# Optimization experiments

Measured on AMD Instinct MI355X. Metric: run time of the kernel, lower is better.

The kernel has to match this reference:

```python
import jax, jax.numpy as jnp
import numpy as np

# Llama-3-8B-ish config + NSA defaults from the adapter
H, KVH, DH = 32, 8, 128
D = H * DH            # 4096 hidden
CB = 16               # compress block size (stride == block -> non-overlapping)
SB = 16               # selection block size
NSEL = 4              # num selected blocks
WIN = 64              # sliding window size
B, S = 1, 1024
NEG = -jnp.finfo(jnp.float32).max


def rope(x):
    # interleaved rotary (rotary_embedding_torch default, theta=10000); x: [b,h,n,d]
    b, h, n, d = x.shape
    inv = 1.0 / (10000.0 ** (jnp.arange(0, d, 2, dtype=jnp.float32) / d))
    ang = jnp.arange(n, dtype=jnp.float32)[:, None] * inv[None, :]      # [n, d/2]
    cos, sin = jnp.cos(ang), jnp.sin(ang)
    xr = x.reshape(b, h, n, d // 2, 2)
    x0, x1 = xr[..., 0], xr[..., 1]
    o0 = x0 * cos - x1 * sin
    o1 = x1 * cos + x0 * sin
    return jnp.stack([o0, o1], axis=-1).reshape(b, h, n, d)


def nsa_forward(hidden_states, w_qkv, w_o, k_pos, v_pos,
                k_w1, k_b1, k_w2, k_b2, v_w1, v_b1, v_w2, v_b2,
                mem_kv, w_gate, b_gate):
    Bq, Sq = hidden_states.shape[:2]
    G = H // KVH
    scale = DH ** -0.5

    qkv = hidden_states @ w_qkv.T
    q, k, v = jnp.split(qkv, [H * DH, H * DH + KVH * DH], axis=-1)
    q = q.reshape(Bq, Sq, H, DH).transpose(0, 2, 1, 3)     # b h s d
    k = k.reshape(Bq, Sq, KVH, DH).transpose(0, 2, 1, 3)   # b kvh s d
    v = v.reshape(Bq, Sq, KVH, DH).transpose(0, 2, 1, 3)

    # ---- branch 1: compressed (coarse) attention ------------------------
    nC = Sq // CB
    kp = jnp.tile(k_pos, (1, nC, 1))[None]                 # intra-block learned positions
    vp = jnp.tile(v_pos, (1, nC, 1))[None]
    ck_in = (k + kp).reshape(Bq, KVH, nC, CB * DH)
    cv_in = (v + vp).reshape(Bq, KVH, nC, CB * DH)
    ck = jax.nn.relu(ck_in @ k_w1.T + k_b1) @ k_w2.T + k_b2   # b kvh nC d
    cv = jax.nn.relu(cv_in @ v_w1.T + v_b1) @ v_w2.T + v_b2
    mem_k = jnp.broadcast_to(mem_kv[0], (Bq, KVH, 1, DH))
    mem_v = jnp.broadcast_to(mem_kv[1], (Bq, KVH, 1, DH))
    ck = jnp.concatenate([mem_k, ck], axis=2)              # b kvh (1+nC) d
    cv = jnp.concatenate([mem_v, cv], axis=2)

    qg = q.reshape(Bq, KVH, G, Sq, DH)
    csim = jnp.einsum('bhgid,bhjd->bhgij', qg, ck) * scale
    ck_seq = jnp.concatenate([jnp.array([-1]), (jnp.arange(nC) + 1) * CB - 1])
    cmask = ck_seq[None, :] < jnp.arange(Sq)[:, None]      # [S, 1+nC], mem always visible
    csim = jnp.where(cmask, csim, NEG)
    c_out = jnp.einsum('bhgij,bhjd->bhgid', jax.nn.softmax(csim, -1), cv)
    c_out = c_out.reshape(Bq, H, Sq, DH)

    # ---- importance scores -> top-k selected blocks ---------------------
    imp = csim[..., 1:].mean(axis=2)                       # mean over grouped q heads: b kvh s nC
    sent = jnp.full(imp.shape[:-1] + (1,), -1e3, imp.dtype)
    imp = jax.nn.softmax(jnp.concatenate([sent, imp], -1), -1)[..., 1:]
    sel_val, sel_idx = jax.lax.top_k(imp, NSEL)            # b kvh s NSEL
    fmask_sel = sel_val > 1e-10

    rq, rk = rope(q), rope(k)

    # ---- branch 2: fine attention over selected + own (block-causal) block
    own = jnp.arange(Sq) // SB
    sel_idx = jnp.concatenate(
        [sel_idx, jnp.broadcast_to(own, (Bq, KVH, Sq))[..., None]], axis=-1)  # b kvh s (NSEL+1)
    nF = Sq // SB
    fk_b = rk.reshape(Bq, KVH, nF, SB, DH)
    fv_b = v.reshape(Bq, KVH, nF, SB, DH)
    bi = jnp.arange(Bq)[:, None, None, None]
    hi = jnp.arange(KVH)[None, :, None, None]
    fk = fk_b[bi, hi, sel_idx].reshape(Bq, KVH, Sq, (NSEL + 1) * SB, DH)
    fv = fv_b[bi, hi, sel_idx].reshape(Bq, KVH, Sq, (NSEL + 1) * SB, DH)

    diag = jnp.arange(SB)[None, :] <= (jnp.arange(Sq) % SB)[:, None]   # [S, SB]
    fmask = jnp.concatenate(
        [jnp.broadcast_to(fmask_sel[..., None], (Bq, KVH, Sq, NSEL, SB)),
         jnp.broadcast_to(diag, (Bq, KVH, Sq, SB))[..., None, :]], axis=3)
    fmask = fmask.reshape(Bq, KVH, 1, Sq, (NSEL + 1) * SB)

    fq = rq.reshape(Bq, KVH, G, Sq, DH)
    fsim = jnp.einsum('bhgid,bhijd->bhgij', fq, fk) * scale
    fsim = jnp.where(fmask, fsim, NEG)
    f_out = jnp.einsum('bhgij,bhijd->bhgid', jax.nn.softmax(fsim, -1), fv)
    f_out = f_out.reshape(Bq, H, Sq, DH)

    # ---- branch 3: sliding window (exact window, look_backward=1) -------
    sk = jnp.repeat(rk, G, axis=1)                          # b H s d
    sv = jnp.repeat(v, G, axis=1)
    nW = Sq // WIN
    sqw = rq.reshape(Bq, H, nW, WIN, DH)
    skw = sk.reshape(Bq, H, nW, WIN, DH)
    svw = sv.reshape(Bq, H, nW, WIN, DH)
    pad5 = ((0, 0), (0, 0), (1, 0), (0, 0), (0, 0))
    skc = jnp.concatenate([jnp.pad(skw, pad5)[:, :, :nW], skw], axis=3)  # prev + own window
    svc = jnp.concatenate([jnp.pad(svw, pad5)[:, :, :nW], svw], axis=3)
    rel = (WIN + jnp.arange(WIN))[:, None] - jnp.arange(2 * WIN)[None, :]  # i_abs - j_abs
    band = (rel >= 0) & (rel <= WIN)
    key_abs = jnp.arange(nW)[:, None] * WIN + jnp.arange(2 * WIN)[None, :] - WIN
    smask = band[None] & (key_abs >= 0)[:, None, :]
    ssim = jnp.einsum('bhwid,bhwjd->bhwij', sqw, skc) * scale
    ssim = jnp.where(smask, ssim, NEG)
    s_out = jnp.einsum('bhwij,bhwjd->bhwid', jax.nn.softmax(ssim, -1), svc)
    s_out = s_out.reshape(Bq, H, Sq, DH)

    # ---- learned 3-way gate + output projection --------------------------
    gates = jax.nn.sigmoid(hidden_states @ w_gate.T + b_gate)
    gates = gates.reshape(Bq, Sq, H, 3).transpose(0, 2, 1, 3)  # b h s 3
    out = gates[..., 0:1] * c_out + gates[..., 1:2] * f_out + gates[..., 2:3] * s_out
    out = out.transpose(0, 2, 1, 3).reshape(Bq, Sq, H * DH)
    return out @ w_o.T


def setup_inputs():
    key = jax.random.key(0)
    ks = jax.random.split(key, 12)
    cdim = CB * DH
    rn = lambda k, shape, s: jax.random.normal(k, shape, dtype=jnp.float32) * s
    return {
        'hidden_states': rn(ks[0], (B, S, D), 1.0),
        'w_qkv': rn(ks[1], (H * DH + 2 * KVH * DH, D), D ** -0.5),
        'w_o': rn(ks[2], (D, H * DH), D ** -0.5),
        'k_pos': rn(ks[3], (KVH, CB, DH), 0.02),
        'v_pos': rn(ks[4], (KVH, CB, DH), 0.02),
        'k_w1': rn(ks[5], (cdim, cdim), cdim ** -0.5),
        'k_b1': jnp.zeros((cdim,), jnp.float32),
        'k_w2': rn(ks[6], (DH, cdim), cdim ** -0.5),
        'k_b2': jnp.zeros((DH,), jnp.float32),
        'v_w1': rn(ks[7], (cdim, cdim), cdim ** -0.5),
        'v_b1': jnp.zeros((cdim,), jnp.float32),
        'v_w2': rn(ks[8], (DH, cdim), cdim ** -0.5),
        'v_b2': jnp.zeros((DH,), jnp.float32),
        'mem_kv': rn(ks[9], (2, KVH, 1, DH), 0.02),
        'w_gate': rn(ks[10], (3 * H, D), 0.02),
        'b_gate': jnp.tile(jnp.array([-2.0, -2.0, 2.0], jnp.float32), H),
    }


def reference(hidden_states, w_qkv, w_o, k_pos, v_pos,
              k_w1, k_b1, k_w2, k_b2, v_w1, v_b1, v_w2, v_b2,
              mem_kv, w_gate, b_gate):
    return nsa_forward(hidden_states, w_qkv, w_o, k_pos, v_pos,
                       k_w1, k_b1, k_w2, k_b2, v_w1, v_b1, v_w2, v_b2,
                       mem_kv, w_gate, b_gate)
```

## Files before the change

kernel.cpp:

```cpp
#include <hip/hip_runtime.h>
#include <hip/hip_bf16.h>

typedef __hip_bfloat16 bf16;
typedef __attribute__((ext_vector_type(8))) short short8;
typedef __attribute__((ext_vector_type(4))) float f32x4;

#define NEGF (-3.402823466e38f)
#define SCALE 0.08838834764831845f

constexpr int S_    = 1024;
constexpr int H_    = 32;
constexpr int KVH_  = 8;
constexpr int DH_   = 128;
constexpr int QKVN  = 6144;
constexpr int NC_   = 64;
constexpr int CD_   = 2048;

__device__ __forceinline__ short f2bf(float x) {
    union { float f; unsigned u; } v; v.f = x;
    unsigned r = v.u + 0x7fffu + ((v.u >> 16) & 1u);
    return (short)(r >> 16);
}
__device__ __forceinline__ float bf2f(short h) {
    union { float f; unsigned u; } v; v.u = ((unsigned)(unsigned short)h) << 16;
    return v.f;
}

#define GLOAD16(gp, lp) __builtin_amdgcn_global_load_lds( \
    (const __attribute__((address_space(1))) unsigned int*)(gp), \
    (__attribute__((address_space(3))) unsigned int*)(lp), 16, 0, 0)

__global__ void split_pair(const float* __restrict__ src, short* __restrict__ h,
                           short* __restrict__ l, long n)
{
    long i = ((long)blockIdx.x * blockDim.x + threadIdx.x) * 8;
    if (i >= n) return;
    float4 a0 = *(const float4*)&src[i];
    float4 a1 = *(const float4*)&src[i + 4];
    float e[8] = {a0.x, a0.y, a0.z, a0.w, a1.x, a1.y, a1.z, a1.w};
    short8 hh, ll;
    #pragma unroll
    for (int j = 0; j < 8; ++j) {
        short hv = f2bf(e[j]); hh[j] = hv; ll[j] = f2bf(e[j] - bf2f(hv));
    }
    *(short8*)&h[i] = hh;
    *(short8*)&l[i] = ll;
}

__global__ __launch_bounds__(64)
void gemm_w64(const short* __restrict__ Ah, const short* __restrict__ Al,
              const short* __restrict__ Bh, const short* __restrict__ Bl,
              float* __restrict__ C, float* __restrict__ Cpart,
              const float* __restrict__ bias,
              int M, int N, int K, int ldc, int k_len, int act)
{
    __shared__ short LA[2][2][2048];
    __shared__ short LB[2][2][2048];
    const int lane = threadIdx.x;
    const int qd = lane >> 4, l16 = lane & 15;
    const int bm = blockIdx.y * 64, bn = blockIdx.x * 64;
    const int kbeg = blockIdx.z * k_len;
    const int kend = (kbeg + k_len < K) ? (kbeg + k_len) : K;

    const int srow = lane >> 2, skq = lane & 3;
    const short* gAh = Ah + (size_t)(bm + srow) * K + skq * 8;
    const short* gAl = Al + (size_t)(bm + srow) * K + skq * 8;
    const short* gBh = Bh + (size_t)(bn + srow) * K + skq * 8;
    const short* gBl = Bl + (size_t)(bn + srow) * K + skq * 8;

    #define STAGE(buf, kk) do {                                         \
        _Pragma("unroll")                                               \
        for (int c = 0; c < 4; ++c) {                                   \
            size_t go = (size_t)c * 16 * K + (kk);                      \
            GLOAD16(gAh + go, &LA[buf][0][c * 512]);                    \
            GLOAD16(gAl + go, &LA[buf][1][c * 512]);                    \
            GLOAD16(gBh + go, &LB[buf][0][c * 512]);                    \
            GLOAD16(gBl + go, &LB[buf][1][c * 512]);                    \
        } } while (0)

    f32x4 zero = {0.f, 0.f, 0.f, 0.f};
    f32x4 acc[4][4];
    #pragma unroll
    for (int i = 0; i < 4; ++i)
        #pragma unroll
        for (int j = 0; j < 4; ++j) acc[i][j] = zero;

    STAGE(0, kbeg);
    int cur = 0;
    for (int k0 = kbeg; k0 < kend; k0 += 32) {
        if (k0 + 32 < kend) {
            STAGE(cur ^ 1, k0 + 32);
            asm volatile("s_waitcnt vmcnt(16)" ::: "memory");
        } else {
            asm volatile("s_waitcnt vmcnt(0)" ::: "memory");
        }
        short8 fah[4], fal[4], fbh[4], fbl[4];
        #pragma unroll
        for (int t = 0; t < 4; ++t) {
            int off = t * 512 + l16 * 32 + qd * 8;
            fah[t] = *(const short8*)&LA[cur][0][off];
            fal[t] = *(const short8*)&LA[cur][1][off];
            fbh[t] = *(const short8*)&LB[cur][0][off];
            fbl[t] = *(const short8*)&LB[cur][1][off];
        }
        __builtin_amdgcn_s_setprio(1);
        #pragma unroll
        for (int t = 0; t < 4; ++t)
            #pragma unroll
            for (int u = 0; u < 4; ++u) {
                acc[t][u] = __builtin_amdgcn_mfma_f32_16x16x32_bf16(fah[t], fbh[u], acc[t][u], 0, 0, 0);
                acc[t][u] = __builtin_amdgcn_mfma_f32_16x16x32_bf16(fah[t], fbl[u], acc[t][u], 0, 0, 0);
                acc[t][u] = __builtin_amdgcn_mfma_f32_16x16x32_bf16(fal[t], fbh[u], acc[t][u], 0, 0, 0);
            }
        __builtin_amdgcn_s_setprio(0);
        cur ^= 1;
    }
    #undef STAGE

    float* dst = Cpart ? (Cpart + (size_t)blockIdx.z * M * ldc) : C;
    #pragma unroll
    for (int t = 0; t < 4; ++t) {
        #pragma unroll
        for (int u = 0; u < 4; ++u) {
            int row0 = bm + t * 16 + qd * 4;
            int col  = bn + u * 16 + l16;
            #pragma unroll
            for (int r = 0; r < 4; ++r) {
                float v = acc[t][u][r];
                if (!Cpart) {
                    if (bias) v += bias[col];
                    if (act == 1) v = fmaxf(v, 0.f);
                    else if (act == 2) v = 1.f / (1.f + expf(-v));
                }
                dst[(size_t)(row0 + r) * ldc + col] = v;
            }
        }
    }
}

__global__ __launch_bounds__(256)
void gemm128(const float* __restrict__ A, const float* __restrict__ B,
             float* __restrict__ C, float* __restrict__ Cpart,
             const float* __restrict__ bias,
             int M, int N, int K, int k_len, int act)
{
    __shared__ float As[16][132];
    __shared__ float Bs[16][132];
    const int tid  = threadIdx.x;
    const int wave = tid >> 6, lane = tid & 63;
    const int wr = wave >> 1, wc = wave & 1;
    const int ro = wr * 64 + (lane >> 3) * 8;
    const int co = wc * 64 + (lane & 7) * 8;
    const int bm = blockIdx.y * 128, bn = blockIdx.x * 128;
    const int z  = blockIdx.z;
    const int kbeg = z * k_len;
    const int lr = tid >> 2;
    const int kq = (tid & 3) * 4;

    float acc[8][8];
    #pragma unroll
    for (int i = 0; i < 8; ++i)
        #pragma unroll
        for (int j = 0; j < 8; ++j) acc[i][j] = 0.f;

    for (int k0 = kbeg; k0 < kbeg + k_len; k0 += 16) {
        #pragma unroll
        for (int h = 0; h < 2; ++h) {
            int r = lr + h * 64;
            float4 av = make_float4(0.f, 0.f, 0.f, 0.f);
            float4 bv = make_float4(0.f, 0.f, 0.f, 0.f);
            if (bm + r < M) av = *(const float4*)&A[(size_t)(bm + r) * K + k0 + kq];
            if (bn + r < N) bv = *(const float4*)&B[(size_t)(bn + r) * K + k0 + kq];
            As[kq + 0][r] = av.x; As[kq + 1][r] = av.y;
            As[kq + 2][r] = av.z; As[kq + 3][r] = av.w;
            Bs[kq + 0][r] = bv.x; Bs[kq + 1][r] = bv.y;
            Bs[kq + 2][r] = bv.z; Bs[kq + 3][r] = bv.w;
        }
        __syncthreads();
        #pragma unroll
        for (int kk = 0; kk < 16; ++kk) {
            float4 a0 = *(const float4*)&As[kk][ro];
            float4 a1 = *(const float4*)&As[kk][ro + 4];
            float4 b0 = *(const float4*)&Bs[kk][co];
            float4 b1 = *(const float4*)&Bs[kk][co + 4];
            float a[8] = {a0.x, a0.y, a0.z, a0.w, a1.x, a1.y, a1.z, a1.w};
            float b[8] = {b0.x, b0.y, b0.z, b0.w, b1.x, b1.y, b1.z, b1.w};
            #pragma unroll
            for (int i = 0; i < 8; ++i)
                #pragma unroll
                for (int j = 0; j < 8; ++j)
                    acc[i][j] += a[i] * b[j];
        }
        __syncthreads();
    }

    if (Cpart) {
        float* P = Cpart + (size_t)z * M * N;
        #pragma unroll
        for (int i = 0; i < 8; ++i) {
            int row = bm + ro + i;
            #pragma unroll
            for (int jq = 0; jq < 2; ++jq) {
                int col = bn + co + jq * 4;
                if (col < N) {
                    float4 v = make_float4(acc[i][jq * 4 + 0], acc[i][jq * 4 + 1],
                                           acc[i][jq * 4 + 2], acc[i][jq * 4 + 3]);
                    *(float4*)&P[(size_t)row * N + col] = v;
                }
            }
        }
    } else {
        #pragma unroll
        for (int i = 0; i < 8; ++i) {
            int row = bm + ro + i;
            #pragma unroll
            for (int jq = 0; jq < 2; ++jq) {
                int col = bn + co + jq * 4;
                if (col < N) {
                    float4 v = make_float4(acc[i][jq * 4 + 0], acc[i][jq * 4 + 1],
                                           acc[i][jq * 4 + 2], acc[i][jq * 4 + 3]);
                    if (bias) {
                        float4 bv = *(const float4*)&bias[col];
                        v.x += bv.x; v.y += bv.y; v.z += bv.z; v.w += bv.w;
                    }
                    if (act == 1) {
                        v.x = fmaxf(v.x, 0.f); v.y = fmaxf(v.y, 0.f);
                        v.z = fmaxf(v.z, 0.f); v.w = fmaxf(v.w, 0.f);
                    } else if (act == 2) {
                        v.x = 1.f / (1.f + expf(-v.x)); v.y = 1.f / (1.f + expf(-v.y));
                        v.z = 1.f / (1.f + expf(-v.z)); v.w = 1.f / (1.f + expf(-v.w));
                    }
                    *(float4*)&C[(size_t)row * N + col] = v;
                }
            }
        }
    }
}

__global__ void reduce_slices(const float* __restrict__ P, float* __restrict__ C,
                              short* __restrict__ Chi, short* __restrict__ Clo,
                              const float* __restrict__ bias,
                              int MN, int N, int KS, int act)
{
    int i4 = blockIdx.x * blockDim.x + threadIdx.x;
    size_t base = (size_t)i4 * 4;
    if (base >= (size_t)MN) return;
    float4 s = *(const float4*)&P[base];
    for (int z = 1; z < KS; ++z) {
        float4 v = *(const float4*)&P[(size_t)z * MN + base];
        s.x += v.x; s.y += v.y; s.z += v.z; s.w += v.w;
    }
    if (bias) {
        int col = (int)(base % N);
        float4 bv = *(const float4*)&bias[col];
        s.x += bv.x; s.y += bv.y; s.z += bv.z; s.w += bv.w;
    }
    if (act == 1) {
        s.x = fmaxf(s.x, 0.f); s.y = fmaxf(s.y, 0.f);
        s.z = fmaxf(s.z, 0.f); s.w = fmaxf(s.w, 0.f);
    } else if (act == 2) {
        s.x = 1.f / (1.f + expf(-s.x)); s.y = 1.f / (1.f + expf(-s.y));
        s.z = 1.f / (1.f + expf(-s.z)); s.w = 1.f / (1.f + expf(-s.w));
    }
    if (Chi) {
        float e[4] = {s.x, s.y, s.z, s.w};
        short4 hh, ll;
        hh.x = f2bf(e[0]); ll.x = f2bf(e[0] - bf2f(hh.x));
        hh.y = f2bf(e[1]); ll.y = f2bf(e[1] - bf2f(hh.y));
        hh.z = f2bf(e[2]); ll.z = f2bf(e[2] - bf2f(hh.z));
        hh.w = f2bf(e[3]); ll.w = f2bf(e[3] - bf2f(hh.w));
        *(short4*)&Chi[base] = hh;
        *(short4*)&Clo[base] = ll;
    } else {
        *(float4*)&C[base] = s;
    }
}

__global__ void build_cin(const float* __restrict__ qkv,
                          const float* __restrict__ k_pos,
                          const float* __restrict__ v_pos,
                          short* __restrict__ ckh, short* __restrict__ ckl,
                          short* __restrict__ cvh, short* __restrict__ cvl)
{
    int idx = blockIdx.x * blockDim.x + threadIdx.x;
    if (idx >= KVH_ * S_ * DH_) return;
    int d = idx & 127;
    int s = (idx >> 7) & 1023;
    int h = idx >> 17;
    int c = s >> 4, t = s & 15;
    float kv = qkv[(size_t)s * QKVN + 4096 + h * DH_ + d];
    float vv = qkv[(size_t)s * QKVN + 5120 + h * DH_ + d];
    size_t row = (size_t)h * NC_ + c;
    size_t col = (size_t)t * DH_ + d;
    float kx = kv + k_pos[(h * 16 + t) * DH_ + d];
    float vx = vv + v_pos[(h * 16 + t) * DH_ + d];
    short kh = f2bf(kx), vh = f2bf(vx);
    ckh[row * CD_ + col] = kh; ckl[row * CD_ + col] = f2bf(kx - bf2f(kh));
    cvh[row * CD_ + col] = vh; cvl[row * CD_ + col] = f2bf(vx - bf2f(vh));
}

__global__ void assemble_c(const float* __restrict__ ckb, const float* __restrict__ cvb,
                           const float* __restrict__ mem_kv,
                           float* __restrict__ ckf, float* __restrict__ cvf)
{
    int idx = blockIdx.x * blockDim.x + threadIdx.x;
    if (idx >= KVH_ * 65 * DH_) return;
    int d = idx & 127;
    int j = (idx >> 7) % 65;
    int h = idx / (65 * DH_);
    if (j == 0) {
        ckf[idx] = mem_kv[(0 * KVH_ + h) * DH_ + d];
        cvf[idx] = mem_kv[(1 * KVH_ + h) * DH_ + d];
    } else {
        ckf[idx] = ckb[((size_t)h * NC_ + (j - 1)) * DH_ + d];
        cvf[idx] = cvb[((size_t)h * NC_ + (j - 1)) * DH_ + d];
    }
}

__global__ void compress_attn(const float* __restrict__ qkv,
                              const float* __restrict__ ckf,
                              const float* __restrict__ cvf,
                              float* __restrict__ cout,
                              int* __restrict__ selidx, int* __restrict__ fsel)
{
    int b = blockIdx.x;
    int s = b & 1023;
    int h = b >> 10;
    int tid = threadIdx.x;
    int wv = tid >> 6;
    __shared__ __align__(16) float qrow[4][128];
    __shared__ float simS[4][65];
    __shared__ float p[4][128];
    __shared__ float redm[2][4], redd[2][4];
    #pragma unroll
    for (int g = 0; g < 4; ++g)
        qrow[g][tid] = qkv[(size_t)s * QKVN + (h * 4 + g) * DH_ + tid];
    __syncthreads();

    float sv[4] = {NEGF, NEGF, NEGF, NEGF};
    if (tid < 65) {
        bool vis = (tid == 0) || (16 * tid - 1 < s);
        if (vis) {
            const float4* kr = (const float4*)(ckf + ((size_t)h * 65 + tid) * DH_);
            float a[4] = {0.f, 0.f, 0.f, 0.f};
            #pragma unroll 4
            for (int d = 0; d < 32; ++d) {
                float4 kq = kr[d];
                #pragma unroll
                for (int g = 0; g < 4; ++g) {
                    float4 qq = *(const float4*)&qrow[g][d * 4];
                    a[g] += kq.x * qq.x + kq.y * qq.y + kq.z * qq.z + kq.w * qq.w;
                }
            }
            #pragma unroll
            for (int g = 0; g < 4; ++g) sv[g] = a[g] * SCALE;
        }
        #pragma unroll
        for (int g = 0; g < 4; ++g) simS[g][tid] = sv[g];
    }

    float mg[4];
    #pragma unroll
    for (int g = 0; g < 4; ++g) mg[g] = sv[g];
    #pragma unroll
    for (int off = 32; off; off >>= 1)
        #pragma unroll
        for (int g = 0; g < 4; ++g) mg[g] = fmaxf(mg[g], __shfl_xor(mg[g], off));
    if ((tid & 63) == 0)
        #pragma unroll
        for (int g = 0; g < 4; ++g) redm[wv][g] = mg[g];
    __syncthreads();
    float e[4];
    #pragma unroll
    for (int g = 0; g < 4; ++g) {
        float m = fmaxf(redm[0][g], redm[1][g]);
        e[g] = (tid < 65) ? expf(sv[g] - m) : 0.f;
        p[g][tid] = e[g];
    }
    __syncthreads();
    #pragma unroll
    for (int off = 32; off; off >>= 1)
        #pragma unroll
        for (int g = 0; g < 4; ++g) e[g] += __shfl_xor(e[g], off);
    if ((tid & 63) == 0)
        #pragma unroll
        for (int g = 0; g < 4; ++g) redd[wv][g] = e[g];
    __syncthreads();
    float inv[4];
    #pragma unroll
    for (int g = 0; g < 4; ++g) inv[g] = 1.f / (redd[0][g] + redd[1][g]);

    if (wv == 1) {
        int j = tid - 64;
        float v = 0.25f * (simS[0][j + 1] + simS[1][j + 1] +
                           simS[2][j + 1] + simS[3][j + 1]);
        float m2 = v;
        #pragma unroll
        for (int off = 32; off; off >>= 1) m2 = fmaxf(m2, __shfl_xor(m2, off));
        m2 = fmaxf(m2, -1e3f);
        float e2 = expf(v - m2);
        float den2 = e2;
        #pragma unroll
        for (int off = 32; off; off >>= 1) den2 += __shfl_xor(den2, off);
        den2 += expf(-1e3f - m2);
        float pv = e2 / den2;
        size_t base5 = ((size_t)h * S_ + s) * 5;
        size_t base4 = ((size_t)h * S_ + s) * 4;
        float cv = pv; int ci = j;
        for (int t = 0; t < 4; ++t) {
            float bv = cv; int bi = ci;
            #pragma unroll
            for (int off = 32; off; off >>= 1) {
                float ov = __shfl_xor(bv, off);
                int   oi = __shfl_xor(bi, off);
                if (ov > bv || (ov == bv && oi < bi)) { bv = ov; bi = oi; }
            }
            if (j == 0) {
                selidx[base5 + t] = bi;
                fsel[base4 + t]   = (bv > 1e-10f) ? 1 : 0;
            }
            if (ci == bi) cv = -1.f;
        }
        if (j == 0) selidx[base5 + 4] = s >> 4;
    }

    float acc[4] = {0.f, 0.f, 0.f, 0.f};
    const float* vbase = cvf + (size_t)h * 65 * DH_ + tid;
    #pragma unroll 4
    for (int j = 0; j < 65; ++j) {
        float v = vbase[(size_t)j * DH_];
        #pragma unroll
        for (int g = 0; g < 4; ++g) acc[g] += p[g][j] * v;
    }
    #pragma unroll
    for (int g = 0; g < 4; ++g)
        cout[(size_t)s * 4096 + (h * 4 + g) * DH_ + tid] = acc[g] * inv[g];
}

__global__ void rope_inplace(float* __restrict__ qkv)
{
    int idx = blockIdx.x * blockDim.x + threadIdx.x;
    const int totq = S_ * H_ * 64;
    const int totk = S_ * KVH_ * 64;
    float* base;
    int p, s;
    if (idx < totq) {
        p = idx & 63; int head = (idx >> 6) & 31; s = idx >> 11;
        base = qkv + (size_t)s * QKVN + head * DH_;
    } else {
        int i2 = idx - totq;
        if (i2 >= totk) return;
        p = i2 & 63; int head = (i2 >> 6) & 7; s = i2 >> 9;
        base = qkv + (size_t)s * QKVN + 4096 + head * DH_;
    }
    float inv = exp2f(-0.2076205060833595f * (float)p);
    float ang = (float)s * inv;
    float c = cosf(ang), sn = sinf(ang);
    float x0 = base[2 * p], x1 = base[2 * p + 1];
    base[2 * p]     = x0 * c - x1 * sn;
    base[2 * p + 1] = x1 * c + x0 * sn;
}

__global__ void fine_attn(const float* __restrict__ qkv,
                          const int* __restrict__ selidx, const int* __restrict__ fsel,
                          float* __restrict__ fout)
{
    int b = blockIdx.x;
    int s = b & 1023;
    int h = b >> 10;
    int tid = threadIdx.x;
    int wv = tid >> 6;
    __shared__ __align__(16) float qrow[4][128];
    __shared__ float p[4][128];
    __shared__ int   blk[5];
    __shared__ int   bvis[5];
    __shared__ float redm[2][4], redd[2][4];
    if (tid < 5) {
        blk[tid]  = selidx[((size_t)h * S_ + s) * 5 + tid];
        bvis[tid] = (tid < 4) ? fsel[((size_t)h * S_ + s) * 4 + tid] : 1;
    }
    #pragma unroll
    for (int g = 0; g < 4; ++g)
        qrow[g][tid] = qkv[(size_t)s * QKVN + (h * 4 + g) * DH_ + tid];
    __syncthreads();

    float sv[4] = {NEGF, NEGF, NEGF, NEGF};
    if (tid < 80) {
        int bi = tid >> 4, t = tid & 15;
        int pos = blk[bi] * 16 + t;
        bool vis = (bi < 4) ? (bvis[bi] != 0) : (t <= (s & 15));
        if (vis) {
            const float4* kr = (const float4*)(qkv + (size_t)pos * QKVN + 4096 + h * DH_);
            float a[4] = {0.f, 0.f, 0.f, 0.f};
            #pragma unroll 4
            for (int d = 0; d < 32; ++d) {
                float4 kq = kr[d];
                #pragma unroll
                for (int g = 0; g < 4; ++g) {
                    float4 qq = *(const float4*)&qrow[g][d * 4];
                    a[g] += kq.x * qq.x + kq.y * qq.y + kq.z * qq.z + kq.w * qq.w;
                }
            }
            #pragma unroll
            for (int g = 0; g < 4; ++g) sv[g] = a[g] * SCALE;
        }
    }

    float mg[4];
    #pragma unroll
    for (int g = 0; g < 4; ++g) mg[g] = sv[g];
    #pragma unroll
    for (int off = 32; off; off >>= 1)
        #pragma unroll
        for (int g = 0; g < 4; ++g) mg[g] = fmaxf(mg[g], __shfl_xor(mg[g], off));
    if ((tid & 63) == 0)
        #pragma unroll
        for (int g = 0; g < 4; ++g) redm[wv][g] = mg[g];
    __syncthreads();
    float e[4];
    #pragma unroll
    for (int g = 0; g < 4; ++g) {
        float m = fmaxf(redm[0][g], redm[1][g]);
        e[g] = (tid < 80) ? expf(sv[g] - m) : 0.f;
        p[g][tid] = e[g];
    }
    __syncthreads();
    #pragma unroll
    for (int off = 32; off; off >>= 1)
        #pragma unroll
        for (int g = 0; g < 4; ++g) e[g] += __shfl_xor(e[g], off);
    if ((tid & 63) == 0)
        #pragma unroll
        for (int g = 0; g < 4; ++g) redd[wv][g] = e[g];
    __syncthreads();
    float inv[4];
    #pragma unroll
    for (int g = 0; g < 4; ++g) inv[g] = 1.f / (redd[0][g] + redd[1][g]);

    float acc[4] = {0.f, 0.f, 0.f, 0.f};
    const float* vbase = qkv + 5120 + h * DH_ + tid;
    #pragma unroll
    for (int bi = 0; bi < 5; ++bi) {
        const float* vb = vbase + (size_t)(blk[bi] * 16) * QKVN;
        #pragma unroll 4
        for (int t = 0; t < 16; ++t) {
            float v = vb[(size_t)t * QKVN];
            #pragma unroll
            for (int g = 0; g < 4; ++g) acc[g] += p[g][bi * 16 + t] * v;
        }
    }
    #pragma unroll
    for (int g = 0; g < 4; ++g)
        fout[(size_t)s * 4096 + (h * 4 + g) * DH_ + tid] = acc[g] * inv[g];
}

__global__ void sliding_attn(const float* __restrict__ qkv, float* __restrict__ sout)
{
    int b = blockIdx.x;
    int s = b & 1023;
    int h = b >> 10;
    int tid = threadIdx.x;
    int wv = tid >> 6;
    __shared__ __align__(16) float qrow[4][128];
    __shared__ float p[4][128];
    __shared__ float redm[2][4], redd[2][4];
    #pragma unroll
    for (int g = 0; g < 4; ++g)
        qrow[g][tid] = qkv[(size_t)s * QKVN + (h * 4 + g) * DH_ + tid];
    __syncthreads();

    float sv[4] = {NEGF, NEGF, NEGF, NEGF};
    if (tid < 65) {
        int pos = s - tid;
        if (pos >= 0) {
            const float4* kr = (const float4*)(qkv + (size_t)pos * QKVN + 4096 + h * DH_);
            float a[4] = {0.f, 0.f, 0.f, 0.f};
            #pragma unroll 4
            for (int d = 0; d < 32; ++d) {
                float4 kq = kr[d];
                #pragma unroll
                for (int g = 0; g < 4; ++g) {
                    float4 qq = *(const float4*)&qrow[g][d * 4];
                    a[g] += kq.x * qq.x + kq.y * qq.y + kq.z * qq.z + kq.w * qq.w;
                }
            }
            #pragma unroll
            for (int g = 0; g < 4; ++g) sv[g] = a[g] * SCALE;
        }
    }

    float mg[4];
    #pragma unroll
    for (int g = 0; g < 4; ++g) mg[g] = sv[g];
    #pragma unroll
    for (int off = 32; off; off >>= 1)
        #pragma unroll
        for (int g = 0; g < 4; ++g) mg[g] = fmaxf(mg[g], __shfl_xor(mg[g], off));
    if ((tid & 63) == 0)
        #pragma unroll
        for (int g = 0; g < 4; ++g) redm[wv][g] = mg[g];
    __syncthreads();
    float e[4];
    #pragma unroll
    for (int g = 0; g < 4; ++g) {
        float m = fmaxf(redm[0][g], redm[1][g]);
        e[g] = (tid < 65) ? expf(sv[g] - m) : 0.f;
        p[g][tid] = e[g];
    }
    __syncthreads();
    #pragma unroll
    for (int off = 32; off; off >>= 1)
        #pragma unroll
        for (int g = 0; g < 4; ++g) e[g] += __shfl_xor(e[g], off);
    if ((tid & 63) == 0)
        #pragma unroll
        for (int g = 0; g < 4; ++g) redd[wv][g] = e[g];
    __syncthreads();
    float inv[4];
    #pragma unroll
    for (int g = 0; g < 4; ++g) inv[g] = 1.f / (redd[0][g] + redd[1][g]);

    float acc[4] = {0.f, 0.f, 0.f, 0.f};
    int lim = (s + 1 < 65) ? (s + 1) : 65;
    const float* vbase = qkv + (size_t)s * QKVN + 5120 + h * DH_ + tid;
    #pragma unroll 4
    for (int j = 0; j < lim; ++j) {
        float v = *(vbase - (size_t)j * QKVN);
        #pragma unroll
        for (int g = 0; g < 4; ++g) acc[g] += p[g][j] * v;
    }
    #pragma unroll
    for (int g = 0; g < 4; ++g)
        sout[(size_t)s * 4096 + (h * 4 + g) * DH_ + tid] = acc[g] * inv[g];
}

__global__ void combine_gate(const float* __restrict__ cout, const float* __restrict__ fout,
                             const float* __restrict__ sout, const float* __restrict__ gates,
                             short* __restrict__ oh, short* __restrict__ ol)
{
    int idx = blockIdx.x * blockDim.x + threadIdx.x;
    if (idx >= S_ * 4096) return;
    int h = (idx >> 7) & 31;
    int s = idx >> 12;
    float g0 = gates[(size_t)s * 96 + h * 3 + 0];
    float g1 = gates[(size_t)s * 96 + h * 3 + 1];
    float g2 = gates[(size_t)s * 96 + h * 3 + 2];
    float v = g0 * cout[idx] + g1 * fout[idx] + g2 * sout[idx];
    short hv = f2bf(v);
    oh[idx] = hv;
    ol[idx] = f2bf(v - bf2f(hv));
}

extern "C" void kernel_launch(void* const* d_in, const int* in_sizes, int n_in,
                              void* d_out, int out_size, void* d_ws, size_t ws_size,
                              hipStream_t stream)
{
    const float* hidden = (const float*)d_in[0];
    const float* w_qkv  = (const float*)d_in[1];
    const float* w_o    = (const float*)d_in[2];
    const float* k_pos  = (const float*)d_in[3];
    const float* v_pos  = (const float*)d_in[4];
    const float* k_w1   = (const float*)d_in[5];
    const float* k_b1   = (const float*)d_in[6];
    const float* k_w2   = (const float*)d_in[7];
    const float* k_b2   = (const float*)d_in[8];
    const float* v_w1   = (const float*)d_in[9];
    const float* v_b1   = (const float*)d_in[10];
    const float* v_w2   = (const float*)d_in[11];
    const float* v_b2   = (const float*)d_in[12];
    const float* mem_kv = (const float*)d_in[13];
    const float* w_gate = (const float*)d_in[14];
    const float* b_gate = (const float*)d_in[15];
    float* out = (float*)d_out;

    float* ws = (float*)d_ws;
    size_t o = 0;
    float* qkv    = ws + o; o += (size_t)S_ * QKVN;
    short* ckin_h = (short*)(ws + o); o += (size_t)512 * CD_ / 2;
    short* ckin_l = (short*)(ws + o); o += (size_t)512 * CD_ / 2;
    short* cvin_h = (short*)(ws + o); o += (size_t)512 * CD_ / 2;
    short* cvin_l = (short*)(ws + o); o += (size_t)512 * CD_ / 2;
    short* h1h    = (short*)(ws + o); o += (size_t)512 * CD_ / 2;
    short* h1l    = (short*)(ws + o); o += (size_t)512 * CD_ / 2;
    float* ckb    = ws + o; o += (size_t)512 * DH_;
    float* cvb    = ws + o; o += (size_t)512 * DH_;
    float* ckf    = ws + o; o += (size_t)KVH_ * 65 * DH_;
    float* cvf    = ws + o; o += (size_t)KVH_ * 65 * DH_;
    float* coutb  = ws + o; o += (size_t)S_ * 4096;
    float* foutb  = ws + o; o += (size_t)S_ * 4096;
    float* soutb  = ws + o; o += (size_t)S_ * 4096;
    float* gatesb = ws + o; o += (size_t)S_ * 96;
    int*   selidx = (int*)(ws + o); o += (size_t)KVH_ * S_ * 5;
    int*   fsel   = (int*)(ws + o); o += (size_t)KVH_ * S_ * 4;
    short* hid_h  = (short*)(ws + o); o += (size_t)S_ * 4096 / 2;
    short* hid_l  = (short*)(ws + o); o += (size_t)S_ * 4096 / 2;
    short* cmb_h  = (short*)(ws + o); o += (size_t)S_ * 4096 / 2;
    short* cmb_l  = (short*)(ws + o); o += (size_t)S_ * 4096 / 2;
    short* wsp_h  = (short*)(ws + o); o += (size_t)QKVN * 4096 / 2;
    short* wsp_l  = (short*)(ws + o); o += (size_t)QKVN * 4096 / 2;

    float* P = foutb;

    {
        long n = (long)S_ * 4096;
        split_pair<<<(int)((n / 8 + 255) / 256), 256, 0, stream>>>(hidden, hid_h, hid_l, n);
        long nw = (long)QKVN * 4096;
        split_pair<<<(int)((nw / 8 + 255) / 256), 256, 0, stream>>>(w_qkv, wsp_h, wsp_l, nw);
    }

    gemm_w64<<<dim3(QKVN / 64, S_ / 64, 1), 64, 0, stream>>>(
        hid_h, hid_l, wsp_h, wsp_l, qkv, nullptr, nullptr,
        S_, QKVN, 4096, QKVN, 4096, 0);

    gemm128<<<dim3(1, S_ / 128, 16), 256, 0, stream>>>(
        hidden, w_gate, nullptr, P, nullptr, S_, 96, 4096, 256, 0);
    reduce_slices<<<(S_ * 96 / 4 + 255) / 256, 256, 0, stream>>>(
        P, gatesb, nullptr, nullptr, b_gate, S_ * 96, 96, 16, 2);

    build_cin<<<(KVH_ * S_ * DH_ + 255) / 256, 256, 0, stream>>>(
        qkv, k_pos, v_pos, ckin_h, ckin_l, cvin_h, cvin_l);

    {
        long nw = (long)CD_ * CD_;
        split_pair<<<(int)((nw / 8 + 255) / 256), 256, 0, stream>>>(k_w1, wsp_h, wsp_l, nw);
    }
    gemm_w64<<<dim3(CD_ / 64, 8, 4), 64, 0, stream>>>(
        ckin_h, ckin_l, wsp_h, wsp_l, nullptr, P, nullptr,
        512, CD_, CD_, CD_, 512, 0);
    reduce_slices<<<(512 * CD_ / 4 + 255) / 256, 256, 0, stream>>>(
        P, nullptr, h1h, h1l, k_b1, 512 * CD_, CD_, 4, 1);
    {
        long nw = (long)DH_ * CD_;
        split_pair<<<(int)((nw / 8 + 255) / 256), 256, 0, stream>>>(k_w2, wsp_h, wsp_l, nw);
    }
    gemm_w64<<<dim3(DH_ / 64, 8, 16), 64, 0, stream>>>(
        h1h, h1l, wsp_h, wsp_l, nullptr, P, nullptr,
        512, DH_, CD_, DH_, 128, 0);
    reduce_slices<<<(512 * DH_ / 4 + 255) / 256, 256, 0, stream>>>(
        P, ckb, nullptr, nullptr, k_b2, 512 * DH_, DH_, 16, 0);

    {
        long nw = (long)CD_ * CD_;
        split_pair<<<(int)((nw / 8 + 255) / 256), 256, 0, stream>>>(v_w1, wsp_h, wsp_l, nw);
    }
    gemm_w64<<<dim3(CD_ / 64, 8, 4), 64, 0, stream>>>(
        cvin_h, cvin_l, wsp_h, wsp_l, nullptr, P, nullptr,
        512, CD_, CD_, CD_, 512, 0);
    reduce_slices<<<(512 * CD_ / 4 + 255) / 256, 256, 0, stream>>>(
        P, nullptr, h1h, h1l, v_b1, 512 * CD_, CD_, 4, 1);
    {
        long nw = (long)DH_ * CD_;
        split_pair<<<(int)((nw / 8 + 255) / 256), 256, 0, stream>>>(v_w2, wsp_h, wsp_l, nw);
    }
    gemm_w64<<<dim3(DH_ / 64, 8, 16), 64, 0, stream>>>(
        h1h, h1l, wsp_h, wsp_l, nullptr, P, nullptr,
        512, DH_, CD_, DH_, 128, 0);
    reduce_slices<<<(512 * DH_ / 4 + 255) / 256, 256, 0, stream>>>(
        P, cvb, nullptr, nullptr, v_b2, 512 * DH_, DH_, 16, 0);

    assemble_c<<<(KVH_ * 65 * DH_ + 255) / 256, 256, 0, stream>>>(ckb, cvb, mem_kv, ckf, cvf);

    compress_attn<<<KVH_ * S_, 128, 0, stream>>>(qkv, ckf, cvf, coutb, selidx, fsel);

    {
        int tot = S_ * H_ * 64 + S_ * KVH_ * 64;
        rope_inplace<<<(tot + 255) / 256, 256, 0, stream>>>(qkv);
    }

    fine_attn<<<KVH_ * S_, 128, 0, stream>>>(qkv, selidx, fsel, foutb);

    sliding_attn<<<KVH_ * S_, 128, 0, stream>>>(qkv, soutb);

    combine_gate<<<(S_ * 4096 + 255) / 256, 256, 0, stream>>>(
        coutb, foutb, soutb, gatesb, cmb_h, cmb_l);

    {
        long nw = (long)4096 * 4096;
        split_pair<<<(int)((nw / 8 + 255) / 256), 256, 0, stream>>>(w_o, wsp_h, wsp_l, nw);
    }
    gemm_w64<<<dim3(4096 / 64, S_ / 64, 1), 64, 0, stream>>>(
        cmb_h, cmb_l, wsp_h, wsp_l, out, nullptr, nullptr,
        S_, 4096, 4096, 4096, 4096, 0);
}
```

Before: 1.060 ms.

## Add 128x128 four-wave bf16x3 GEMM with split-K and swizzle LDS in gemm_w64

Adds a new 256-thread GEMM kernel with 128x128 tiles for the bf16 hi/lo three-product emulated fp32 matmuls. The QKV, compressor first-layer and output projections now use it with split-K plus a reduction pass, and the second-layer split-K factor is doubled. It also XOR-swizzles the LDS layout in the 64-wide GEMM to cut bank conflicts. The new kernel is single-buffered with two barriers per K step and adds extra partial-sum traffic and reduction launches. The workspace front is reused as the output partial buffer, which could alias other live buffers.

Measured after the change: 1.051 ms. About the same (-0.8%).

```diff
diff --git a/kernel.cpp b/kernel.cpp
--- a/kernel.cpp
+++ b/kernel.cpp
@@ -47,6 +47,96 @@
     *(short8*)&l[i] = ll;
 }
 
+__global__ __launch_bounds__(256)
+void gemm_bf3(const short* __restrict__ Ah, const short* __restrict__ Al,
+              const short* __restrict__ Bh, const short* __restrict__ Bl,
+              float* __restrict__ C, float* __restrict__ Cpart,
+              const float* __restrict__ bias,
+              int M, int N, int K, int ldc, int k_len, int act)
+{
+    __shared__ short LAh[4096];
+    __shared__ short LAl[4096];
+    __shared__ short LBh[4096];
+    __shared__ short LBl[4096];
+    const int tid  = threadIdx.x;
+    const int lane = tid & 63, wave = tid >> 6;
+    const int wr = wave >> 1, wc = wave & 1;
+    const int qd = lane >> 4, l16 = lane & 15;
+    const int bm = blockIdx.y * 128, bn = blockIdx.x * 128;
+    const int kbeg = blockIdx.z * k_len;
+    const int kend = (kbeg + k_len < K) ? (kbeg + k_len) : K;
+
+    const short* gA[2][2];
+    const short* gB[2][2];
+    int cbase[2];
+    #pragma unroll
+    for (int c = 0; c < 2; ++c) {
+        int cell = (wave * 2 + c) * 64 + lane;
+        int row = cell & 127, kq = cell >> 7;
+        size_t oa = (size_t)(bm + row) * K + kq * 8;
+        size_t ob = (size_t)(bn + row) * K + kq * 8;
+        gA[c][0] = Ah + oa; gA[c][1] = Al + oa;
+        gB[c][0] = Bh + ob; gB[c][1] = Bl + ob;
+        cbase[c] = (wave * 2 + c) * 512;
+    }
+
+    f32x4 zero = {0.f, 0.f, 0.f, 0.f};
+    f32x4 acc[4][4];
+    #pragma unroll
+    for (int i = 0; i < 4; ++i)
+        #pragma unroll
+        for (int j = 0; j < 4; ++j) acc[i][j] = zero;
+
+    for (int k0 = kbeg; k0 < kend; k0 += 32) {
+        #pragma unroll
+        for (int c = 0; c < 2; ++c) {
+            GLOAD16(gA[c][0] + k0, &LAh[cbase[c]]);
+            GLOAD16(gA[c][1] + k0, &LAl[cbase[c]]);
+            GLOAD16(gB[c][0] + k0, &LBh[cbase[c]]);
+            GLOAD16(gB[c][1] + k0, &LBl[cbase[c]]);
+        }
+        __syncthreads();
+
+        short8 fah[4], fal[4], fbh[4], fbl[4];
+        #pragma unroll
+        for (int t = 0; t < 4; ++t) {
+            int ca = (qd * 128 + wr * 64 + t * 16 + l16) * 8;
+            int cb = (qd * 128 + wc * 64 + t * 16 + l16) * 8;
+            fah[t] = *(const short8*)&LAh[ca]; fal[t] = *(const short8*)&LAl[ca];
+            fbh[t] = *(const short8*)&LBh[cb]; fbl[t] = *(const short8*)&LBl[cb];
+        }
+        #pragma unroll
+        for (int i = 0; i < 4; ++i)
+            #pragma unroll
+            for (int j = 0; j < 4; ++j) {
+                acc[i][j] = __builtin_amdgcn_mfma_f32_16x16x32_bf16(fah[i], fbh[j], acc[i][j], 0, 0, 0);
+                acc[i][j] = __builtin_amdgcn_mfma_f32_16x16x32_bf16(fah[i], fbl[j], acc[i][j], 0, 0, 0);
+                acc[i][j] = __builtin_amdgcn_mfma_f32_16x16x32_bf16(fal[i], fbh[j], acc[i][j], 0, 0, 0);
+            }
+        __syncthreads();
+    }
+
+    float* dst = Cpart ? (Cpart + (size_t)blockIdx.z * M * ldc) : C;
+    #pragma unroll
+    for (int i = 0; i < 4; ++i) {
+        #pragma unroll
+        for (int j = 0; j < 4; ++j) {
+            int row0 = bm + wr * 64 + i * 16 + qd * 4;
+            int col  = bn + wc * 64 + j * 16 + l16;
+            #pragma unroll
+            for (int r = 0; r < 4; ++r) {
+                float v = acc[i][j][r];
+                if (!Cpart) {
+                    if (bias) v += bias[col];
+                    if (act == 1) v = fmaxf(v, 0.f);
+                    else if (act == 2) v = 1.f / (1.f + expf(-v));
+                }
+                dst[(size_t)(row0 + r) * ldc + col] = v;
+            }
+        }
+    }
+}
+
 __global__ __launch_bounds__(64)
 void gemm_w64(const short* __restrict__ Ah, const short* __restrict__ Al,
               const short* __restrict__ Bh, const short* __restrict__ Bl,
@@ -62,7 +152,8 @@
     const int kbeg = blockIdx.z * k_len;
     const int kend = (kbeg + k_len < K) ? (kbeg + k_len) : K;
 
-    const int srow = lane >> 2, skq = lane & 3;
+    const int srow = lane >> 2;
+    const int skq  = (lane & 3) ^ ((lane >> 3) & 3);
     const short* gAh = Ah + (size_t)(bm + srow) * K + skq * 8;
     const short* gAl = Al + (size_t)(bm + srow) * K + skq * 8;
     const short* gBh = Bh + (size_t)(bn + srow) * K + skq * 8;
@@ -85,6 +176,8 @@
         #pragma unroll
         for (int j = 0; j < 4; ++j) acc[i][j] = zero;
 
+    const int pA = qd ^ ((l16 >> 1) & 3);
+
     STAGE(0, kbeg);
     int cur = 0;
     for (int k0 = kbeg; k0 < kend; k0 += 32) {
@@ -97,7 +190,7 @@
         short8 fah[4], fal[4], fbh[4], fbl[4];
         #pragma unroll
         for (int t = 0; t < 4; ++t) {
-            int off = t * 512 + l16 * 32 + qd * 8;
+            int off = t * 512 + l16 * 32 + pA * 8;
             fah[t] = *(const short8*)&LA[cur][0][off];
             fal[t] = *(const short8*)&LA[cur][1][off];
             fbh[t] = *(const short8*)&LB[cur][0][off];
@@ -699,7 +792,9 @@
     short* wsp_h  = (short*)(ws + o); o += (size_t)QKVN * 4096 / 2;
     short* wsp_l  = (short*)(ws + o); o += (size_t)QKVN * 4096 / 2;
 
-    float* P = foutb;
+    float* Pq = coutb;
+    float* P  = foutb;
+    float* Po = ws;
 
     {
         long n = (long)S_ * 4096;
@@ -708,9 +803,11 @@
         split_pair<<<(int)((nw / 8 + 255) / 256), 256, 0, stream>>>(w_qkv, wsp_h, wsp_l, nw);
     }
 
-    gemm_w64<<<dim3(QKVN / 64, S_ / 64, 1), 64, 0, stream>>>(
-        hid_h, hid_l, wsp_h, wsp_l, qkv, nullptr, nullptr,
-        S_, QKVN, 4096, QKVN, 4096, 0);
+    gemm_bf3<<<dim3(QKVN / 128, S_ / 128, 2), 256, 0, stream>>>(
+        hid_h, hid_l, wsp_h, wsp_l, nullptr, Pq, nullptr,
+        S_, QKVN, 4096, QKVN, 2048, 0);
+    reduce_slices<<<(S_ * QKVN / 4 + 255) / 256, 256, 0, stream>>>(
+        Pq, qkv, nullptr, nullptr, nullptr, S_ * QKVN, QKVN, 2, 0);
 
     gemm128<<<dim3(1, S_ / 128, 16), 256, 0, stream>>>(
         hidden, w_gate, nullptr, P, nullptr, S_, 96, 4096, 256, 0);
@@ -724,39 +821,39 @@
         long nw = (long)CD_ * CD_;
         split_pair<<<(int)((nw / 8 + 255) / 256), 256, 0, stream>>>(k_w1, wsp_h, wsp_l, nw);
     }
-    gemm_w64<<<dim3(CD_ / 64, 8, 4), 64, 0, stream>>>(
+    gemm_bf3<<<dim3(CD_ / 128, 4, 8), 256, 0, stream>>>(
         ckin_h, ckin_l, wsp_h, wsp_l, nullptr, P, nullptr,
-        512, CD_, CD_, CD_, 512, 0);
+        512, CD_, CD_, CD_, 256, 0);
     reduce_slices<<<(512 * CD_ / 4 + 255) / 256, 256, 0, stream>>>(
-        P, nullptr, h1h, h1l, k_b1, 512 * CD_, CD_, 4, 1);
+        P, nullptr, h1h, h1l, k_b1, 512 * CD_, CD_, 8, 1);
     {
         long nw = (long)DH_ * CD_;
         split_pair<<<(int)((nw / 8 + 255) / 256), 256, 0, stream>>>(k_w2, wsp_h, wsp_l, nw);
     }
-    gemm_w64<<<dim3(DH_ / 64, 8, 16), 64, 0, stream>>>(
+    gemm_w64<<<dim3(DH_ / 64, 8, 32), 64, 0, stream>>>(
         h1h, h1l, wsp_h, wsp_l, nullptr, P, nullptr,
-        512, DH_, CD_, DH_, 128, 0);
+        512, DH_, CD_, DH_, 64, 0);
     reduce_slices<<<(512 * DH_ / 4 + 255) / 256, 256, 0, stream>>>(
-        P, ckb, nullptr, nullptr, k_b2, 512 * DH_, DH_, 16, 0);
+        P, ckb, nullptr, nullptr, k_b2, 512 * DH_, DH_, 32, 0);
 
     {
         long nw = (long)CD_ * CD_;
         split_pair<<<(int)((nw / 8 + 255) / 256), 256, 0, stream>>>(v_w1, wsp_h, wsp_l, nw);
     }
-    gemm_w64<<<dim3(CD_ / 64, 8, 4), 64, 0, stream>>>(
+    gemm_bf3<<<dim3(CD_ / 128, 4, 8), 256, 0, stream>>>(
         cvin_h, cvin_l, wsp_h, wsp_l, nullptr, P, nullptr,
-        512, CD_, CD_, CD_, 512, 0);
+        512, CD_, CD_, CD_, 256, 0);
     reduce_slices<<<(512 * CD_ / 4 + 255) / 256, 256, 0, stream>>>(
-        P, nullptr, h1h, h1l, v_b1, 512 * CD_, CD_, 4, 1);
+        P, nullptr, h1h, h1l, v_b1, 512 * CD_, CD_, 8, 1);
     {
         long nw = (long)DH_ * CD_;
         split_pair<<<(int)((nw / 8 + 255) / 256), 256, 0, stream>>>(v_w2, wsp_h, wsp_l, nw);
     }
-    gemm_w64<<<dim3(DH_ / 64, 8, 16), 64, 0, stream>>>(
+    gemm_w64<<<dim3(DH_ / 64, 8, 32), 64, 0, stream>>>(
         h1h, h1l, wsp_h, wsp_l, nullptr, P, nullptr,
-        512, DH_, CD_, DH_, 128, 0);
+        512, DH_, CD_, DH_, 64, 0);
     reduce_slices<<<(512 * DH_ / 4 + 255) / 256, 256, 0, stream>>>(
-        P, cvb, nullptr, nullptr, v_b2, 512 * DH_, DH_, 16, 0);
+        P, cvb, nullptr, nullptr, v_b2, 512 * DH_, DH_, 32, 0);
 
     assemble_c<<<(KVH_ * 65 * DH_ + 255) / 256, 256, 0, stream>>>(ckb, cvb, mem_kv, ckf, cvf);
 
@@ -778,7 +875,9 @@
         long nw = (long)4096 * 4096;
         split_pair<<<(int)((nw / 8 + 255) / 256), 256, 0, stream>>>(w_o, wsp_h, wsp_l, nw);
     }
-    gemm_w64<<<dim3(4096 / 64, S_ / 64, 1), 64, 0, stream>>>(
-        cmb_h, cmb_l, wsp_h, wsp_l, out, nullptr, nullptr,
-        S_, 4096, 4096, 4096, 4096, 0);
-}
+    gemm_bf3<<<dim3(4096 / 128, S_ / 128, 4), 256, 0, stream>>>(
+        cmb_h, cmb_l, wsp_h, wsp_l, nullptr, Po, nullptr,
+        S_, 4096, 4096, 4096, 1024, 0);
+    reduce_slices<<<(S_ * 4096 / 4 + 255) / 256, 256, 0, stream>>>(
+        Po, out, nullptr, nullptr, nullptr, S_ * 4096, 4096, 4, 0);
+}
```
